# Kernel tuning notes

Measured on AMD Instinct MI355X. Metric: run time of the kernel, lower is better.

Reference implementation:

```python
import jax, jax.numpy as jnp
import numpy as np

# Model config (matches init_kwargs)
L, B, S, D, H, HKV, HD, FF, V = 2, 1, 2048, 2048, 16, 4, 128, 5632, 32000
EPS = 1e-5
ROPE_BASE = 10000.0


def setup_inputs() -> dict:
    key = jax.random.key(0)
    ks = jax.random.split(key, 13)
    s = 0.02  # init scale keeps activations/softmax numerically sane
    return {
        "idx": jax.random.randint(ks[0], (B, S), 0, V, dtype=jnp.int32),
        "embed": jax.random.normal(ks[1], (V, D), jnp.float32) * s,
        "wq": jax.random.normal(ks[2], (L, D, D), jnp.float32) * s,
        "wk": jax.random.normal(ks[3], (L, D, HKV * HD), jnp.float32) * s,
        "wv": jax.random.normal(ks[4], (L, D, HKV * HD), jnp.float32) * s,
        "wo": jax.random.normal(ks[5], (L, D, D), jnp.float32) * s,
        "ln1_g": jnp.ones((L, D), jnp.float32),
        "ln2_g": jnp.ones((L, D), jnp.float32),
        "w_gate": jax.random.normal(ks[6], (L, D, FF), jnp.float32) * s,
        "w_up": jax.random.normal(ks[7], (L, D, FF), jnp.float32) * s,
        "w_down": jax.random.normal(ks[8], (L, FF, D), jnp.float32) * s,
        "final_g": jnp.ones((D,), jnp.float32),
        "lm_head": jax.random.normal(ks[9], (V, D), jnp.float32) * s,
    }


def _rope_cos_sin(seq_len, n_elem, base=ROPE_BASE):
    inv = 1.0 / base ** (jnp.arange(0, n_elem, 2, dtype=jnp.float32)[: n_elem // 2] / n_elem)
    f = jnp.outer(jnp.arange(seq_len, dtype=jnp.float32), inv)  # [S, HD/2]
    return jnp.cos(f), jnp.sin(f)


def _apply_rope(x, cos, sin):
    # x: [B, S, h, HD]; split last dim into halves (matches torch reshape(...,2,-1))
    d2 = x.shape[-1] // 2
    x1, x2 = x[..., :d2], x[..., d2:]
    c = cos[None, :, None, :]
    s = sin[None, :, None, :]
    return jnp.concatenate([x1 * c - x2 * s, x2 * c + x1 * s], axis=-1)


def _rmsnorm(x, g, eps=EPS):
    return x * jax.lax.rsqrt(jnp.mean(x * x, axis=-1, keepdims=True) + eps) * g


def _forward(idx, embed, wq, wk, wv, wo, ln1_g, ln2_g, w_gate, w_up, w_down, final_g, lm_head):
    cos, sin = _rope_cos_sin(S, HD)
    # NOTE: the original uses a MULTIPLICATIVE bool mask on scores (scores * mask),
    # zeroing (not -inf'ing) future positions before softmax. Replicated faithfully.
    mask = jnp.tril(jnp.ones((S, S), jnp.float32))
    rep = H // HKV
    scale = 1.0 / np.sqrt(HD).astype(np.float32)

    x = embed[idx]  # [B, S, D]

    def layer(x, p):
        lwq, lwk, lwv, lwo, g1, g2, lwg, lwu, lwd = p
        h = _rmsnorm(x, g1)
        q = (h @ lwq).reshape(B, S, H, HD)
        k = (h @ lwk).reshape(B, S, HKV, HD)
        v = (h @ lwv).reshape(B, S, HKV, HD)
        q = _apply_rope(q, cos, sin)
        k = _apply_rope(k, cos, sin)
        k = jnp.repeat(k, rep, axis=2)  # GQA repeat_interleave over heads
        v = jnp.repeat(v, rep, axis=2)
        scores = jnp.einsum("bqhd,bkhd->bhqk", q, k) * scale * mask
        attn = jax.nn.softmax(scores, axis=-1)
        y = jnp.einsum("bhqk,bkhd->bqhd", attn, v).reshape(B, S, D) @ lwo
        x = x + y
        h2 = _rmsnorm(x, g2)
        x = x + (jax.nn.silu(h2 @ lwu) * (h2 @ lwg)) @ lwd
        return x, None

    x, _ = jax.lax.scan(layer, x, (wq, wk, wv, wo, ln1_g, ln2_g, w_gate, w_up, w_down))
    return _rmsnorm(x, final_g) @ lm_head.T  # [B, S, V]


def reference(idx, embed, wq, wk, wv, wo, ln1_g, ln2_g, w_gate, w_up, w_down, final_g, lm_head):
    return _forward(idx, embed, wq, wk, wv, wo, ln1_g, ln2_g, w_gate, w_up, w_down, final_g, lm_head)
```

## Files before the change

kernel.cpp:

```cpp
#include <hip/hip_runtime.h>

#define SQ     2048
#define DMODEL 2048
#define NHEAD  16
#define NKV    4
#define HDIM   128
#define FFDIM  5632
#define VOCAB  32000
#define NLAYER 2
#define EPSV   1e-5f

typedef __bf16 bf16;
typedef __bf16 bf16x4 __attribute__((ext_vector_type(4)));
typedef __bf16 bf16x8 __attribute__((ext_vector_type(8)));
typedef float  f32x4  __attribute__((ext_vector_type(4)));

enum { EP_STOREF = 0, EP_ADD = 2, EP_STOREB = 3, EP_QKV = 6, EP_GLU = 7 };

#define GLD(gp, lp) __builtin_amdgcn_global_load_lds( \
    (const __attribute__((address_space(1))) void*)(gp), \
    (__attribute__((address_space(3))) void*)(lp), 16, 0, 0)

#define MFMA16(a, b, c) __builtin_amdgcn_mfma_f32_16x16x32_bf16(a, b, c, 0, 0, 0)

#define FENCE() __builtin_amdgcn_sched_barrier(0)
#define PH_BAR() do { FENCE(); __builtin_amdgcn_s_barrier(); FENCE(); } while (0)

#define XCD_SWZ(TM)                                                        \
  const int GM  = (int)gridDim.x;                                          \
  const int nwg = GM * (int)gridDim.y;                                     \
  const int bid = (int)blockIdx.y * GM + (int)blockIdx.x;                  \
  const int q8  = nwg >> 3, r8 = nwg & 7;                                  \
  const int xcd = bid & 7, rnk = bid >> 3;                                 \
  const int swz = ((xcd < r8) ? xcd * (q8 + 1)                             \
                              : r8 * (q8 + 1) + (xcd - r8) * q8) + rnk;    \
  const int m0  = (swz % GM) * (TM);                                       \
  const int n0  = (swz / GM) * (TM == 256 ? 256 : 128);

template<int EPI, int NBUF>
__global__ __launch_bounds__(256, NBUF == 2 ? 2 : 1)
void gemm128(const bf16* __restrict__ A, const bf16* __restrict__ B,
             void* __restrict__ C, const void* __restrict__ Cin,
             bf16* __restrict__ C2, bf16* __restrict__ C3,
             int K, int lda, int ldb, int ldc)
{
  __shared__ bf16 As[NBUF][128 * 64];
  __shared__ bf16 Bs[NBUF][128 * 64];

  const int tid  = (int)threadIdx.x;
  const int lane = tid & 63;
  const int wave = tid >> 6;
  const int wm   = wave >> 1, wn = wave & 1;

  XCD_SWZ(128)

  const int nkt  = K >> 6;
  const int srow = lane >> 3;
  const long sxcol = (long)(((lane & 7) ^ (lane >> 3)) * 8);
  const int colc = lane & 15;
  const int g4   = lane >> 4;

  auto stage = [&](int t, int buf) {
    if (t < nkt) {
      const long kc = (long)t * 64 + sxcol;
      bf16* dA = As[buf];
      bf16* dB = Bs[buf];
      #pragma unroll
      for (int c = 0; c < 4; ++c) {
        const int chunk = wave * 4 + c;
        const int row   = chunk * 8 + srow;
        GLD(A + (long)(m0 + row) * lda + kc, dA + chunk * 512);
        GLD(B + (long)(n0 + row) * ldb + kc, dB + chunk * 512);
      }
    }
  };

  stage(0, 0);
  if (NBUF == 3) stage(1, 1);

  f32x4 acc[4][4] = {};
  int wb = (NBUF == 3) ? 2 : 1;
  int rb = 0;

  for (int t = 0; t < nkt; ++t) {
    if (NBUF == 2) {
      stage(t + 1, wb);
      wb ^= 1;
      FENCE();
      if (t + 1 < nkt) asm volatile("s_waitcnt vmcnt(8)" ::: "memory");
      else             asm volatile("s_waitcnt vmcnt(0)" ::: "memory");
    } else {
      stage(t + 2, wb);
      wb = (wb == 2) ? 0 : wb + 1;
      FENCE();
      if (t + 2 < nkt)      asm volatile("s_waitcnt vmcnt(16)" ::: "memory");
      else if (t + 1 < nkt) asm volatile("s_waitcnt vmcnt(8)"  ::: "memory");
      else                  asm volatile("s_waitcnt vmcnt(0)"  ::: "memory");
    }
    PH_BAR();
    const char* Ab = (const char*)As[rb];
    const char* Bb = (const char*)Bs[rb];
    rb = (NBUF == 2) ? (rb ^ 1) : ((rb == 2) ? 0 : rb + 1);
    #pragma unroll
    for (int kk = 0; kk < 2; ++kk) {
      bf16x8 af[4], bv[4];
      #pragma unroll
      for (int m = 0; m < 4; ++m) {
        const int r = wm * 64 + m * 16 + colc;
        af[m] = *(const bf16x8*)(Ab + r * 128 + (((kk * 4 + g4) ^ (r & 7)) * 16));
      }
      #pragma unroll
      for (int n = 0; n < 4; ++n) {
        const int r = wn * 64 + n * 16 + colc;
        bv[n] = *(const bf16x8*)(Bb + r * 128 + (((kk * 4 + g4) ^ (r & 7)) * 16));
      }
      #pragma unroll
      for (int m = 0; m < 4; ++m)
        #pragma unroll
        for (int n = 0; n < 4; ++n)
          acc[m][n] = MFMA16(af[m], bv[n], acc[m][n]);
    }
    PH_BAR();
  }

  #pragma unroll
  for (int m = 0; m < 4; ++m) {
    const int gr0 = m0 + wm * 64 + m * 16 + g4 * 4;
    #pragma unroll
    for (int n = 0; n < 4; ++n) {
      const int gc = n0 + wn * 64 + n * 16 + colc;
      if (EPI == EP_QKV) {
        if (n0 < 2048) {
          #pragma unroll
          for (int r = 0; r < 4; ++r)
            ((bf16*)C)[(long)(gr0 + r) * DMODEL + gc] = (bf16)acc[m][n][r];
        } else if (n0 < 2560) {
          #pragma unroll
          for (int r = 0; r < 4; ++r)
            C2[(long)(gr0 + r) * 512 + (gc - 2048)] = (bf16)acc[m][n][r];
        } else {
          bf16x4 pk = { (bf16)acc[m][n][0], (bf16)acc[m][n][1],
                        (bf16)acc[m][n][2], (bf16)acc[m][n][3] };
          *(bf16x4*)(C3 + (long)(gc - 2560) * SQ + gr0) = pk;
        }
      } else if (EPI == EP_GLU) {
        #pragma unroll
        for (int r = 0; r < 4; ++r) {
          const float v = acc[m][n][r];
          const float o = __shfl_xor(v, 1);
          if ((colc & 1) == 0) {
            const float res = (o / (1.0f + __expf(-o))) * v;
            ((bf16*)C)[(long)(gr0 + r) * ldc + (gc >> 1)] = (bf16)res;
          }
        }
      } else {
        #pragma unroll
        for (int r = 0; r < 4; ++r) {
          const long off = (long)(gr0 + r) * ldc + gc;
          const float v = acc[m][n][r];
          if (EPI == EP_STOREF)      ((float*)C)[off] = v;
          else if (EPI == EP_ADD)    ((float*)C)[off] = ((const float*)Cin)[off] + v;
          else if (EPI == EP_STOREB) ((bf16*)C)[off] = (bf16)v;
        }
      }
    }
  }
}

template<int EPI>
__global__ __launch_bounds__(512, 2)
void gemm256(const bf16* __restrict__ A, const bf16* __restrict__ B,
             void* __restrict__ C, const void* __restrict__ Cin,
             int K, int lda, int ldb, int ldc)
{
  __shared__ bf16 smem[2][4][128 * 64];

  const int tid  = (int)threadIdx.x;
  const int lane = tid & 63;
  const int wave = tid >> 6;
  const int wm   = wave >> 2;
  const int wn   = wave & 3;

  XCD_SWZ(256)

  const int nkt  = K >> 6;
  const int srow = lane >> 3;
  const long sxcol = (long)(((lane & 7) ^ (lane >> 3)) * 8);
  const int frow = lane & 15;
  const int ph0  = ((     (lane >> 4)) ^ (lane & 7)) * 16;
  const int ph1  = ((4 + (lane >> 4)) ^ (lane & 7)) * 16;

  auto stageA = [&](int tile, int half) {
    if (tile < nkt) {
      const long kc = (long)tile * 64 + sxcol;
      #pragma unroll
      for (int i = 0; i < 2; ++i)
        GLD(A + (long)(m0 + half * 128 + wave * 16 + i * 8 + srow) * lda + kc,
            smem[tile & 1][half] + (wave * 16 + i * 8) * 64);
    }
  };
  auto stageB = [&](int tile, int half) {
    if (tile < nkt) {
      const long kc = (long)tile * 64 + sxcol;
      #pragma unroll
      for (int i = 0; i < 2; ++i)
        GLD(B + (long)(n0 + half * 128 + wave * 16 + i * 8 + srow) * ldb + kc,
            smem[tile & 1][2 + half] + (wave * 16 + i * 8) * 64);
    }
  };

  stageB(0, 0); stageB(0, 1); stageA(0, 0); stageA(0, 1);
  asm volatile("s_waitcnt vmcnt(4)" ::: "memory");
  stageB(1, 0); stageB(1, 1); stageA(1, 0);
  asm volatile("s_waitcnt vmcnt(6)" ::: "memory");
  PH_BAR();

  f32x4 acc[8][4] = {};

  for (int t = 0; t < nkt; ++t) {
    const int bsel = t & 1;
    const char* Asl = (const char*)smem[bsel][wm];
    const char* Bsl = (const char*)smem[bsel][2 + (wn >> 1)];
    const int brow = (wn & 1) * 64;

    bf16x8 ar[4][2], b0f[2][2], b1f[2][2];

    #pragma unroll
    for (int mr = 0; mr < 4; ++mr) {
      ar[mr][0] = *(const bf16x8*)(Asl + (mr * 16 + frow) * 128 + ph0);
      ar[mr][1] = *(const bf16x8*)(Asl + (mr * 16 + frow) * 128 + ph1);
    }
    #pragma unroll
    for (int nc = 0; nc < 2; ++nc) {
      b0f[nc][0] = *(const bf16x8*)(Bsl + (brow + nc * 16 + frow) * 128 + ph0);
      b0f[nc][1] = *(const bf16x8*)(Bsl + (brow + nc * 16 + frow) * 128 + ph1);
    }
    stageA(t + 1, 1);
    PH_BAR();
    __builtin_amdgcn_s_setprio(1);
    #pragma unroll
    for (int mr = 0; mr < 4; ++mr)
      #pragma unroll
      for (int nc = 0; nc < 2; ++nc) {
        acc[mr][nc] = MFMA16(ar[mr][0], b0f[nc][0], acc[mr][nc]);
        acc[mr][nc] = MFMA16(ar[mr][1], b0f[nc][1], acc[mr][nc]);
      }
    __builtin_amdgcn_s_setprio(0);
    PH_BAR();

    #pragma unroll
    for (int nc = 0; nc < 2; ++nc) {
      b1f[nc][0] = *(const bf16x8*)(Bsl + (brow + (2 + nc) * 16 + frow) * 128 + ph0);
      b1f[nc][1] = *(const bf16x8*)(Bsl + (brow + (2 + nc) * 16 + frow) * 128 + ph1);
    }
    PH_BAR();
    __builtin_amdgcn_s_setprio(1);
    #pragma unroll
    for (int mr = 0; mr < 4; ++mr)
      #pragma unroll
      for (int nc = 0; nc < 2; ++nc) {
        acc[mr][2 + nc] = MFMA16(ar[mr][0], b1f[nc][0], acc[mr][2 + nc]);
        acc[mr][2 + nc] = MFMA16(ar[mr][1], b1f[nc][1], acc[mr][2 + nc]);
      }
    __builtin_amdgcn_s_setprio(0);
    PH_BAR();

    #pragma unroll
    for (int mr = 0; mr < 4; ++mr) {
      ar[mr][0] = *(const bf16x8*)(Asl + ((4 + mr) * 16 + frow) * 128 + ph0);
      ar[mr][1] = *(const bf16x8*)(Asl + ((4 + mr) * 16 + frow) * 128 + ph1);
    }
    stageB(t + 2, 0); stageB(t + 2, 1);
    PH_BAR();
    __builtin_amdgcn_s_setprio(1);
    #pragma unroll
    for (int mr = 0; mr < 4; ++mr)
      #pragma unroll
      for (int nc = 0; nc < 2; ++nc) {
        acc[4 + mr][nc] = MFMA16(ar[mr][0], b0f[nc][0], acc[4 + mr][nc]);
        acc[4 + mr][nc] = MFMA16(ar[mr][1], b0f[nc][1], acc[4 + mr][nc]);
      }
    __builtin_amdgcn_s_setprio(0);
    PH_BAR();

    stageA(t + 2, 0);
    PH_BAR();
    __builtin_amdgcn_s_setprio(1);
    #pragma unroll
    for (int mr = 0; mr < 4; ++mr)
      #pragma unroll
      for (int nc = 0; nc < 2; ++nc) {
        acc[4 + mr][2 + nc] = MFMA16(ar[mr][0], b1f[nc][0], acc[4 + mr][2 + nc]);
        acc[4 + mr][2 + nc] = MFMA16(ar[mr][1], b1f[nc][1], acc[4 + mr][2 + nc]);
      }
    __builtin_amdgcn_s_setprio(0);
    FENCE();
    if (t + 2 < nkt) asm volatile("s_waitcnt vmcnt(6)" ::: "memory");
    else             asm volatile("s_waitcnt vmcnt(0)" ::: "memory");
    PH_BAR();
  }

  #pragma unroll
  for (int mr = 0; mr < 8; ++mr) {
    const int gr0 = m0 + wm * 128 + mr * 16 + (lane >> 4) * 4;
    #pragma unroll
    for (int nc = 0; nc < 4; ++nc) {
      const int gc = n0 + wn * 64 + nc * 16 + (lane & 15);
      #pragma unroll
      for (int r = 0; r < 4; ++r) {
        const long off = (long)(gr0 + r) * ldc + gc;
        const float v = acc[mr][nc][r];
        if (EPI == EP_STOREF)      ((float*)C)[off] = v;
        else if (EPI == EP_STOREB) ((bf16*)C)[off] = (bf16)v;
      }
    }
  }
}

__global__ __launch_bounds__(256, 1)
void flash_attn(const bf16* __restrict__ qb, const bf16* __restrict__ kb,
                const bf16* __restrict__ vT, const float* __restrict__ suffPc,
                bf16* __restrict__ yb, float scale)
{
  __shared__ bf16 Ks[128 * 128];
  __shared__ bf16 Vs[128 * 128];
  __shared__ bf16 Ps[128 * 136];

  const int tid  = (int)threadIdx.x;
  const int lane = tid & 63;
  const int w    = tid >> 6;
  const int qt   = (int)blockIdx.x;
  const int h    = (int)blockIdx.y;
  const int kvh  = h >> 2;

  const int l15 = lane & 15;
  const int g4  = lane >> 4;

  bf16x8 qf[2][4];
  #pragma unroll
  for (int m = 0; m < 2; ++m)
    #pragma unroll
    for (int ks = 0; ks < 4; ++ks)
      qf[m][ks] = *(const bf16x8*)(qb + (long)(qt * 128 + w * 32 + m * 16 + l15) * DMODEL
                                   + h * HDIM + ks * 32 + g4 * 8);

  f32x4 acc_o[2][8] = {};
  float den[2][4] = {};

  const bf16* Kg = kb + (long)kvh * HDIM;
  const bf16* Vg = vT + (long)(kvh * HDIM) * SQ;

  for (int j = 0; j <= qt; ++j) {
    const bool diag = (j == qt);
    PH_BAR();

    #pragma unroll
    for (int i = 0; i < 8; ++i) {
      const int rb = w * 32 + i * 4;
      const int r  = rb + g4;
      GLD(Kg + (long)(j * 128 + r) * 512 + ((l15 ^ (r & 7)) * 8), Ks + rb * 128);
    }
    #pragma unroll
    for (int i = 0; i < 8; ++i) {
      const int rb = w * 32 + i * 4;
      const int r  = rb + g4;
      GLD(Vg + (long)r * SQ + j * 128 + ((l15 ^ (r & 7)) * 8), Vs + rb * 128);
    }
    asm volatile("s_waitcnt vmcnt(8)" ::: "memory");
    PH_BAR();

    f32x4 acc_s[2][8] = {};
    #pragma unroll
    for (int ks = 0; ks < 4; ++ks) {
      bf16x8 kf[8];
      #pragma unroll
      for (int n = 0; n < 8; ++n) {
        const int kr = n * 16 + l15;
        kf[n] = *(const bf16x8*)((const char*)Ks + kr * 256 + (((ks * 4 + g4) ^ (kr & 7)) * 16));
      }
      #pragma unroll
      for (int m = 0; m < 2; ++m)
        #pragma unroll
        for (int n = 0; n < 8; ++n)
          acc_s[m][n] = MFMA16(qf[m][ks], kf[n], acc_s[m][n]);
    }

    float rs[2][4] = {};
    #pragma unroll
    for (int m = 0; m < 2; ++m)
      #pragma unroll
      for (int n = 0; n < 8; ++n) {
        const int kc = n * 16 + l15;
        #pragma unroll
        for (int r = 0; r < 4; ++r) {
          const int qlr = w * 32 + m * 16 + g4 * 4 + r;
          float p = __expf(acc_s[m][n][r] * scale);
          if (diag && kc > qlr) p = 1.0f;
          rs[m][r] += p;
          Ps[(w * 32 + m * 16 + g4 * 4 + r) * 136 + kc] = (bf16)p;
        }
      }
    #pragma unroll
    for (int m = 0; m < 2; ++m)
      #pragma unroll
      for (int r = 0; r < 4; ++r) {
        float v = rs[m][r];
        v += __shfl_xor(v, 1); v += __shfl_xor(v, 2);
        v += __shfl_xor(v, 4); v += __shfl_xor(v, 8);
        den[m][r] += v;
      }

    asm volatile("s_waitcnt vmcnt(0) lgkmcnt(0)" ::: "memory");
    PH_BAR();

    #pragma unroll
    for (int ks = 0; ks < 4; ++ks) {
      bf16x8 pa[2], vf[8];
      #pragma unroll
      for (int m = 0; m < 2; ++m)
        pa[m] = *(const bf16x8*)((const char*)Ps + (w * 32 + m * 16 + l15) * 272
                                 + ks * 64 + g4 * 16);
      #pragma unroll
      for (int n = 0; n < 8; ++n) {
        const int dr = n * 16 + l15;
        vf[n] = *(const bf16x8*)((const char*)Vs + dr * 256 + (((ks * 4 + g4) ^ (dr & 7)) * 16));
      }
      #pragma unroll
      for (int m = 0; m < 2; ++m)
        #pragma unroll
        for (int n = 0; n < 8; ++n)
          acc_o[m][n] = MFMA16(pa[m], vf[n], acc_o[m][n]);
    }
  }

  float denf[2][4];
  #pragma unroll
  for (int m = 0; m < 2; ++m)
    #pragma unroll
    for (int r = 0; r < 4; ++r)
      denf[m][r] = den[m][r] + 128.0f * (15 - qt);

  #pragma unroll
  for (int n = 0; n < 8; ++n) {
    const float t = suffPc[((kvh << 4) + qt) * 128 + n * 16 + l15];
    #pragma unroll
    for (int m = 0; m < 2; ++m)
      #pragma unroll
      for (int r = 0; r < 4; ++r) {
        const float y = (acc_o[m][n][r] + t) / denf[m][r];
        yb[(long)(qt * 128 + w * 32 + m * 16 + g4 * 4 + r) * DMODEL
           + h * HDIM + n * 16 + l15] = (bf16)y;
      }
  }
}

__global__ __launch_bounds__(128)
void vchunksum(const bf16* __restrict__ vT, float* __restrict__ chunkS)
{
  const int kvh = (int)blockIdx.x;
  const int c   = (int)blockIdx.y;
  const int d   = (int)threadIdx.x;
  const bf16* row = vT + (long)(kvh * HDIM + d) * SQ + c * 128;
  float s = 0.f;
  #pragma unroll
  for (int r = 0; r < 16; ++r) {
    bf16x8 v = *(const bf16x8*)(row + r * 8);
    #pragma unroll
    for (int e = 0; e < 8; ++e) s += (float)v[e];
  }
  chunkS[(kvh * 16 + c) * 128 + d] = s;
}

__global__ __launch_bounds__(128)
void vsuffscan(const float* __restrict__ chunkS, float* __restrict__ suffPc)
{
  const int kvh = (int)blockIdx.x;
  const int d   = (int)threadIdx.x;
  float a = 0.f;
  for (int c = 15; c >= 0; --c) {
    suffPc[(kvh * 16 + c) * 128 + d] = a;
    a += chunkS[(kvh * 16 + c) * 128 + d];
  }
}

__global__ __launch_bounds__(256)
void transpose_cvt3(const float* __restrict__ s0, bf16* __restrict__ d0, int N0, int L0,
                    const float* __restrict__ s1, bf16* __restrict__ d1, int N1, int L1,
                    const float* __restrict__ s2, bf16* __restrict__ d2, int N2, int L2,
                    int K)
{
  const float* src; bf16* dst; int N, L;
  if (blockIdx.z == 0)      { src = s0; dst = d0; N = N0; L = L0; }
  else if (blockIdx.z == 1) { src = s1; dst = d1; N = N1; L = L1; }
  else                      { src = s2; dst = d2; N = N2; L = L2; }
  if (!src) return;
  const int n0 = (int)blockIdx.x * 32; if (n0 >= N) return;
  const int k0 = (int)blockIdx.y * 32;
  __shared__ float t[32][33];
  const int tr = (int)threadIdx.x >> 3;
  const int tc = ((int)threadIdx.x & 7) * 4;
  f32x4 v = *(const f32x4*)(src + (long)(k0 + tr) * N + n0 + tc);
  t[tr][tc] = v[0]; t[tr][tc + 1] = v[1]; t[tr][tc + 2] = v[2]; t[tr][tc + 3] = v[3];
  __syncthreads();
  bf16x4 b = { (bf16)t[tc][tr], (bf16)t[tc + 1][tr], (bf16)t[tc + 2][tr], (bf16)t[tc + 3][tr] };
  *(bf16x4*)(dst + (long)(n0 + tr) * L + k0 + tc) = b;
}

__global__ __launch_bounds__(256)
void cvt_bf16_kernel(const float* __restrict__ in, bf16* __restrict__ out, int nvec)
{
  const int i = (int)(blockIdx.x * 256 + threadIdx.x);
  if (i < nvec) {
    f32x4 v = ((const f32x4*)in)[i];
    bf16x4 b = { (bf16)v[0], (bf16)v[1], (bf16)v[2], (bf16)v[3] };
    ((bf16x4*)out)[i] = b;
  }
}

__global__ __launch_bounds__(256)
void rmsnorm_kernel(bf16* __restrict__ out, const float* __restrict__ in, const float* __restrict__ g)
{
  const int row = (int)blockIdx.x;
  const float* x = in + (long)row * DMODEL;
  bf16* o = out + (long)row * DMODEL;
  const int tid = (int)threadIdx.x;
  f32x4 v0 = *(const f32x4*)(x + tid * 4);
  f32x4 v1 = *(const f32x4*)(x + tid * 4 + 1024);
  float ss = v0[0]*v0[0] + v0[1]*v0[1] + v0[2]*v0[2] + v0[3]*v0[3]
           + v1[0]*v1[0] + v1[1]*v1[1] + v1[2]*v1[2] + v1[3]*v1[3];
  #pragma unroll
  for (int o_ = 32; o_; o_ >>= 1) ss += __shfl_xor(ss, o_);
  __shared__ float sm[4];
  if ((tid & 63) == 0) sm[tid >> 6] = ss;
  __syncthreads();
  ss = sm[0] + sm[1] + sm[2] + sm[3];
  const float r = 1.0f / sqrtf(ss * (1.0f / DMODEL) + EPSV);
  f32x4 g0 = *(const f32x4*)(g + tid * 4);
  f32x4 g1 = *(const f32x4*)(g + tid * 4 + 1024);
  bf16x4 o0, o1;
  #pragma unroll
  for (int j = 0; j < 4; ++j) { o0[j] = (bf16)(v0[j] * r * g0[j]); o1[j] = (bf16)(v1[j] * r * g1[j]); }
  *(bf16x4*)(o + tid * 4) = o0;
  *(bf16x4*)(o + tid * 4 + 1024) = o1;
}

__global__ void rope_tables(float* cosT, float* sinT)
{
  const int s = (int)blockIdx.x;
  const int i = (int)threadIdx.x;
  const double inv = pow(10000.0, -(double)i / 64.0);
  const double f = (double)s * inv;
  cosT[s * 64 + i] = (float)cos(f);
  sinT[s * 64 + i] = (float)sin(f);
}

__global__ __launch_bounds__(256)
void rope_both(bf16* __restrict__ qb, bf16* __restrict__ kb,
               const float* __restrict__ cosT, const float* __restrict__ sinT)
{
  const int blk = (int)blockIdx.x;
  bf16* buf; int nh, stride, t;
  if (blk < 8192) { buf = qb; nh = NHEAD; stride = DMODEL; t = blk * 256 + (int)threadIdx.x; }
  else            { buf = kb; nh = NKV;   stride = 512;    t = (blk - 8192) * 256 + (int)threadIdx.x; }
  const int per = nh * 64;
  const int s = t / per;
  const int r = t - s * per;
  const int h = r >> 6;
  const int i = r & 63;
  bf16* b = buf + (long)s * stride + h * HDIM;
  const float c  = cosT[s * 64 + i];
  const float sn = sinT[s * 64 + i];
  const float x1 = (float)b[i];
  const float x2 = (float)b[64 + i];
  b[i]      = (bf16)(x1 * c - x2 * sn);
  b[64 + i] = (bf16)(x2 * c + x1 * sn);
}

__global__ __launch_bounds__(256)
void embed_gather(f32x4* x, const f32x4* embed, const int* idx)
{
  const int t = (int)(blockIdx.x * 256 + threadIdx.x);
  const int s = t >> 9;
  const int c = t & 511;
  x[t] = embed[(long)idx[s] * 512 + c];
}

extern "C" void kernel_launch(void* const* d_in, const int* in_sizes, int n_in,
                              void* d_out, int out_size, void* d_ws, size_t ws_size,
                              hipStream_t stream)
{
  (void)in_sizes; (void)n_in; (void)out_size;
  const int*   idx   = (const int*)  d_in[0];
  const float* embed = (const float*)d_in[1];
  const float* wq    = (const float*)d_in[2];
  const float* wk    = (const float*)d_in[3];
  const float* wv    = (const float*)d_in[4];
  const float* wo    = (const float*)d_in[5];
  const float* ln1g  = (const float*)d_in[6];
  const float* ln2g  = (const float*)d_in[7];
  const float* wgate = (const float*)d_in[8];
  const float* wup   = (const float*)d_in[9];
  const float* wdown = (const float*)d_in[10];
  const float* fing  = (const float*)d_in[11];
  const float* lmh   = (const float*)d_in[12];
  float* out = (float*)d_out;

  char* wp = (char*)d_ws;
  auto alloc = [&](size_t bytes) { char* p = wp; wp += (bytes + 255) & ~(size_t)255; return p; };
  float* cosT   = (float*)alloc((size_t)SQ * 64 * 4);
  float* sinT   = (float*)alloc((size_t)SQ * 64 * 4);
  float* suffPc = (float*)alloc((size_t)NKV * 16 * 128 * 4);
  float* chunkS = (float*)alloc((size_t)NKV * 16 * 128 * 4);
  float* x      = (float*)alloc((size_t)SQ * DMODEL * 4);
  bf16*  h      = (bf16*) alloc((size_t)SQ * DMODEL * 2);
  bf16*  qb     = (bf16*) alloc((size_t)SQ * DMODEL * 2);
  bf16*  kb     = (bf16*) alloc((size_t)SQ * 512 * 2);
  bf16*  vT     = (bf16*) alloc((size_t)512 * SQ * 2);
  bf16*  ffb    = (bf16*) alloc((size_t)SQ * FFDIM * 2);
  size_t used  = (size_t)(wp - (char*)d_ws);
  bf16*  wbuf  = (bf16*)wp;
  size_t avail = ws_size - used;

  bf16* yb = qb;
  const float scale = 0.08838834764831845f;

  rope_tables<<<SQ, 64, 0, stream>>>(cosT, sinT);
  embed_gather<<<(SQ * 512) / 256, 256, 0, stream>>>((f32x4*)x, (const f32x4*)embed, idx);

  for (int l = 0; l < NLAYER; ++l) {
    const float* lwq = wq    + (long)l * DMODEL * DMODEL;
    const float* lwk = wk    + (long)l * DMODEL * 512;
    const float* lwv = wv    + (long)l * DMODEL * 512;
    const float* lwo = wo    + (long)l * DMODEL * DMODEL;
    const float* lwg = wgate + (long)l * DMODEL * FFDIM;
    const float* lwu = wup   + (long)l * DMODEL * FFDIM;
    const float* lwd = wdown + (long)l * FFDIM * DMODEL;

    rmsnorm_kernel<<<SQ, 256, 0, stream>>>(h, x, ln1g + l * DMODEL);

    transpose_cvt3<<<dim3(64, 64, 3), 256, 0, stream>>>(
        lwq, wbuf, DMODEL, DMODEL,
        lwk, wbuf + (long)2048 * DMODEL, 512, DMODEL,
        lwv, wbuf + (long)2560 * DMODEL, 512, DMODEL, DMODEL);
    gemm128<EP_QKV, 2><<<dim3(16, 24), 256, 0, stream>>>(
        h, wbuf, qb, nullptr, kb, vT, DMODEL, DMODEL, DMODEL, 0);

    vchunksum<<<dim3(NKV, 16), 128, 0, stream>>>(vT, chunkS);
    vsuffscan<<<NKV, 128, 0, stream>>>(chunkS, suffPc);
    rope_both<<<8192 + 2048, 256, 0, stream>>>(qb, kb, cosT, sinT);

    flash_attn<<<dim3(16, NHEAD), 256, 0, stream>>>(qb, kb, vT, suffPc, yb, scale);

    transpose_cvt3<<<dim3(64, 64, 1), 256, 0, stream>>>(
        lwo, wbuf, DMODEL, DMODEL,
        nullptr, nullptr, 0, 0, nullptr, nullptr, 0, 0, DMODEL);
    gemm128<EP_ADD, 3><<<dim3(16, 16), 256, 0, stream>>>(
        yb, wbuf, x, x, nullptr, nullptr, DMODEL, DMODEL, DMODEL, DMODEL);

    rmsnorm_kernel<<<SQ, 256, 0, stream>>>(h, x, ln2g + l * DMODEL);

    transpose_cvt3<<<dim3(176, 64, 2), 256, 0, stream>>>(
        lwg, wbuf, FFDIM, 2 * DMODEL,
        lwu, wbuf + DMODEL, FFDIM, 2 * DMODEL,
        nullptr, nullptr, 0, 0, DMODEL);
    gemm128<EP_GLU, 2><<<dim3(16, 88), 256, 0, stream>>>(
        h, wbuf, ffb, nullptr, nullptr, nullptr, DMODEL, DMODEL, DMODEL, FFDIM);

    transpose_cvt3<<<dim3(64, 176, 1), 256, 0, stream>>>(
        lwd, wbuf, DMODEL, FFDIM,
        nullptr, nullptr, 0, 0, nullptr, nullptr, 0, 0, FFDIM);
    gemm128<EP_ADD, 3><<<dim3(16, 16), 256, 0, stream>>>(
        ffb, wbuf, x, x, nullptr, nullptr, FFDIM, FFDIM, FFDIM, DMODEL);
  }

  rmsnorm_kernel<<<SQ, 256, 0, stream>>>(h, x, fing);

  long chunkRows = (long)(avail / ((size_t)DMODEL * 2)) & ~255L;
  if (chunkRows > VOCAB) chunkRows = VOCAB;
  for (long c0 = 0; c0 < VOCAB; c0 += chunkRows) {
    const long rows = (VOCAB - c0 < chunkRows) ? (VOCAB - c0) : chunkRows;
    const int  nvec = (int)(rows * DMODEL / 4);
    cvt_bf16_kernel<<<(nvec + 255) / 256, 256, 0, stream>>>(lmh + c0 * DMODEL, wbuf, nvec);
    gemm256<EP_STOREF><<<dim3(8, (int)(rows / 256)), 512, 0, stream>>>(
        h, wbuf, out + c0, nullptr, DMODEL, DMODEL, DMODEL, VOCAB);
  }
}
```

Baseline: 1.234 ms.

## Fuse RoPE into QKV GEMM epilogue and reschedule lm_head A-tile prefetch

The standalone rope_both kernel is removed. RoPE is now applied in the QKV GEMM epilogue: the B-fragment column mapping is interleaved so each thread holds both halves (i and i+64) of a head dimension pair, and it rotates them using cos/sin tables before storing Q and K. This saves a kernel launch and a full read-modify-write pass over Q and K, at the cost of extra epilogue arithmetic and table loads inside the GEMM. Separately, the gemm256 pipeline now issues both A halves of the next-next tile together with adjusted vmcnt waits, which changes how loads overlap with MFMA work.

```diff
diff --git a/kernel.cpp b/kernel.cpp
--- a/kernel.cpp
+++ b/kernel.cpp
@@ -42,6 +42,7 @@
 void gemm128(const bf16* __restrict__ A, const bf16* __restrict__ B,
              void* __restrict__ C, const void* __restrict__ Cin,
              bf16* __restrict__ C2, bf16* __restrict__ C3,
+             const float* __restrict__ cosT, const float* __restrict__ sinT,
              int K, int lda, int ldb, int ldc)
 {
   __shared__ bf16 As[NBUF][128 * 64];
@@ -111,7 +112,7 @@
       }
       #pragma unroll
       for (int n = 0; n < 4; ++n) {
-        const int r = wn * 64 + n * 16 + colc;
+        const int r = n * 32 + wn * 16 + colc;
         bv[n] = *(const bf16x8*)(Bb + r * 128 + (((kk * 4 + g4) ^ (r & 7)) * 16));
       }
       #pragma unroll
@@ -123,26 +124,46 @@
     PH_BAR();
   }
 
+  if (EPI == EP_QKV && n0 < 2560) {
+    #pragma unroll
+    for (int m = 0; m < 4; ++m) {
+      const int gr0 = m0 + wm * 64 + m * 16 + g4 * 4;
+      #pragma unroll
+      for (int n = 0; n < 2; ++n) {
+        const int i   = n * 32 + wn * 16 + colc;
+        const int gc1 = n0 + i;
+        #pragma unroll
+        for (int r = 0; r < 4; ++r) {
+          const int row = gr0 + r;
+          const float c  = cosT[row * 64 + i];
+          const float sn = sinT[row * 64 + i];
+          const float x1 = acc[m][n][r];
+          const float x2 = acc[m][n + 2][r];
+          const float y1 = x1 * c - x2 * sn;
+          const float y2 = x2 * c + x1 * sn;
+          if (n0 < 2048) {
+            bf16* q = (bf16*)C + (long)row * DMODEL;
+            q[gc1] = (bf16)y1; q[gc1 + 64] = (bf16)y2;
+          } else {
+            bf16* k = C2 + (long)row * 512 + (gc1 - 2048);
+            k[0] = (bf16)y1; k[64] = (bf16)y2;
+          }
+        }
+      }
+    }
+    return;
+  }
+
   #pragma unroll
   for (int m = 0; m < 4; ++m) {
     const int gr0 = m0 + wm * 64 + m * 16 + g4 * 4;
     #pragma unroll
     for (int n = 0; n < 4; ++n) {
-      const int gc = n0 + wn * 64 + n * 16 + colc;
+      const int gc = n0 + n * 32 + wn * 16 + colc;
       if (EPI == EP_QKV) {
-        if (n0 < 2048) {
-          #pragma unroll
-          for (int r = 0; r < 4; ++r)
-            ((bf16*)C)[(long)(gr0 + r) * DMODEL + gc] = (bf16)acc[m][n][r];
-        } else if (n0 < 2560) {
-          #pragma unroll
-          for (int r = 0; r < 4; ++r)
-            C2[(long)(gr0 + r) * 512 + (gc - 2048)] = (bf16)acc[m][n][r];
-        } else {
-          bf16x4 pk = { (bf16)acc[m][n][0], (bf16)acc[m][n][1],
-                        (bf16)acc[m][n][2], (bf16)acc[m][n][3] };
-          *(bf16x4*)(C3 + (long)(gc - 2560) * SQ + gr0) = pk;
-        }
+        bf16x4 pk = { (bf16)acc[m][n][0], (bf16)acc[m][n][1],
+                      (bf16)acc[m][n][2], (bf16)acc[m][n][3] };
+        *(bf16x4*)(C3 + (long)(gc - 2560) * SQ + gr0) = pk;
       } else if (EPI == EP_GLU) {
         #pragma unroll
         for (int r = 0; r < 4; ++r) {
@@ -210,9 +231,8 @@
   };
 
   stageB(0, 0); stageB(0, 1); stageA(0, 0); stageA(0, 1);
-  asm volatile("s_waitcnt vmcnt(4)" ::: "memory");
-  stageB(1, 0); stageB(1, 1); stageA(1, 0);
-  asm volatile("s_waitcnt vmcnt(6)" ::: "memory");
+  stageB(1, 0); stageB(1, 1); stageA(1, 0); stageA(1, 1);
+  asm volatile("s_waitcnt vmcnt(8)" ::: "memory");
   PH_BAR();
 
   f32x4 acc[8][4] = {};
@@ -235,7 +255,6 @@
       b0f[nc][0] = *(const bf16x8*)(Bsl + (brow + nc * 16 + frow) * 128 + ph0);
       b0f[nc][1] = *(const bf16x8*)(Bsl + (brow + nc * 16 + frow) * 128 + ph1);
     }
-    stageA(t + 1, 1);
     PH_BAR();
     __builtin_amdgcn_s_setprio(1);
     #pragma unroll
@@ -283,7 +302,7 @@
     __builtin_amdgcn_s_setprio(0);
     PH_BAR();
 
-    stageA(t + 2, 0);
+    stageA(t + 2, 0); stageA(t + 2, 1);
     PH_BAR();
     __builtin_amdgcn_s_setprio(1);
     #pragma unroll
@@ -295,7 +314,7 @@
       }
     __builtin_amdgcn_s_setprio(0);
     FENCE();
-    if (t + 2 < nkt) asm volatile("s_waitcnt vmcnt(6)" ::: "memory");
+    if (t + 2 < nkt) asm volatile("s_waitcnt vmcnt(8)" ::: "memory");
     else             asm volatile("s_waitcnt vmcnt(0)" ::: "memory");
     PH_BAR();
   }
@@ -555,28 +574,6 @@
 }
 
 __global__ __launch_bounds__(256)
-void rope_both(bf16* __restrict__ qb, bf16* __restrict__ kb,
-               const float* __restrict__ cosT, const float* __restrict__ sinT)
-{
-  const int blk = (int)blockIdx.x;
-  bf16* buf; int nh, stride, t;
-  if (blk < 8192) { buf = qb; nh = NHEAD; stride = DMODEL; t = blk * 256 + (int)threadIdx.x; }
-  else            { buf = kb; nh = NKV;   stride = 512;    t = (blk - 8192) * 256 + (int)threadIdx.x; }
-  const int per = nh * 64;
-  const int s = t / per;
-  const int r = t - s * per;
-  const int h = r >> 6;
-  const int i = r & 63;
-  bf16* b = buf + (long)s * stride + h * HDIM;
-  const float c  = cosT[s * 64 + i];
-  const float sn = sinT[s * 64 + i];
-  const float x1 = (float)b[i];
-  const float x2 = (float)b[64 + i];
-  b[i]      = (bf16)(x1 * c - x2 * sn);
-  b[64 + i] = (bf16)(x2 * c + x1 * sn);
-}
-
-__global__ __launch_bounds__(256)
 void embed_gather(f32x4* x, const f32x4* embed, const int* idx)
 {
   const int t = (int)(blockIdx.x * 256 + threadIdx.x);
@@ -643,11 +640,10 @@
         lwk, wbuf + (long)2048 * DMODEL, 512, DMODEL,
         lwv, wbuf + (long)2560 * DMODEL, 512, DMODEL, DMODEL);
     gemm128<EP_QKV, 2><<<dim3(16, 24), 256, 0, stream>>>(
-        h, wbuf, qb, nullptr, kb, vT, DMODEL, DMODEL, DMODEL, 0);
+        h, wbuf, qb, nullptr, kb, vT, cosT, sinT, DMODEL, DMODEL, DMODEL, 0);
 
     vchunksum<<<dim3(NKV, 16), 128, 0, stream>>>(vT, chunkS);
     vsuffscan<<<NKV, 128, 0, stream>>>(chunkS, suffPc);
-    rope_both<<<8192 + 2048, 256, 0, stream>>>(qb, kb, cosT, sinT);
 
     flash_attn<<<dim3(16, NHEAD), 256, 0, stream>>>(qb, kb, vT, suffPc, yb, scale);
 
@@ -655,7 +651,8 @@
         lwo, wbuf, DMODEL, DMODEL,
         nullptr, nullptr, 0, 0, nullptr, nullptr, 0, 0, DMODEL);
     gemm128<EP_ADD, 3><<<dim3(16, 16), 256, 0, stream>>>(
-        yb, wbuf, x, x, nullptr, nullptr, DMODEL, DMODEL, DMODEL, DMODEL);
+        yb, wbuf, x, x, nullptr, nullptr, nullptr, nullptr,
+        DMODEL, DMODEL, DMODEL, DMODEL);
 
     rmsnorm_kernel<<<SQ, 256, 0, stream>>>(h, x, ln2g + l * DMODEL);
 
@@ -664,13 +661,15 @@
         lwu, wbuf + DMODEL, FFDIM, 2 * DMODEL,
         nullptr, nullptr, 0, 0, DMODEL);
     gemm128<EP_GLU, 2><<<dim3(16, 88), 256, 0, stream>>>(
-        h, wbuf, ffb, nullptr, nullptr, nullptr, DMODEL, DMODEL, DMODEL, FFDIM);
+        h, wbuf, ffb, nullptr, nullptr, nullptr, nullptr, nullptr,
+        DMODEL, DMODEL, DMODEL, FFDIM);
 
     transpose_cvt3<<<dim3(64, 176, 1), 256, 0, stream>>>(
         lwd, wbuf, DMODEL, FFDIM,
         nullptr, nullptr, 0, 0, nullptr, nullptr, 0, 0, FFDIM);
     gemm128<EP_ADD, 3><<<dim3(16, 16), 256, 0, stream>>>(
-        ffb, wbuf, x, x, nullptr, nullptr, FFDIM, FFDIM, FFDIM, DMODEL);
+        ffb, wbuf, x, x, nullptr, nullptr, nullptr, nullptr,
+        FFDIM, FFDIM, FFDIM, DMODEL);
   }
 
   rmsnorm_kernel<<<SQ, 256, 0, stream>>>(h, x, fing);
```

Result: slower. 1.261 ms (+2.2%).
